# Performance work log

Measured on AMD Instinct MI355X. Metric: run time of the kernel, lower is better.

The kernel has to match this reference:

```python
import jax, jax.numpy as jnp
import numpy as np
from jax import lax

B, L = 4, 1024
D_MODEL, D_STATE, D_CONV = 512, 16, 4
D_INNER = 2 * D_MODEL          # expand=2
DT_RANK = D_MODEL // 16        # ceil(512/16)=32
K_EXPERTS = 2                  # num_experts_per_token; only first k experts are used
EPS = 1e-5


def setup_inputs() -> dict:
    key = jax.random.key(0)
    ks = jax.random.split(key, 14)
    def n(k, shape, scale=0.02):
        return jax.random.normal(k, shape, jnp.float32) * scale
    # Mamba S4D-real init for A: A_log = log(1..d_state) broadcast over channels
    A_log = jnp.log(jnp.broadcast_to(jnp.arange(1, D_STATE + 1, dtype=jnp.float32), (D_INNER, D_STATE)))
    return {
        "x": jax.random.normal(ks[0], (B, L, D_MODEL), jnp.float32),
        "in_proj_w": n(ks[1], (2 * D_INNER, D_MODEL)),
        "conv_w": n(ks[2], (D_INNER, 1, D_CONV), 0.1),
        "conv_b": n(ks[3], (D_INNER,), 0.1),
        "x_proj_w": n(ks[4], (DT_RANK + 2 * D_STATE, D_INNER)),
        "dt_proj_w": n(ks[5], (D_INNER, DT_RANK), 0.1),
        "dt_proj_b": n(ks[6], (D_INNER,), 0.1),
        "A_log": A_log,
        "D_skip": jnp.ones((D_INNER,), jnp.float32),
        "out_proj_w": n(ks[7], (D_MODEL, D_INNER)),
        "moe_w1": n(ks[8], (K_EXPERTS, 2 * D_MODEL, D_MODEL)),
        "moe_b1": n(ks[9], (K_EXPERTS, 2 * D_MODEL)),
        "moe_w2": n(ks[10], (K_EXPERTS, D_MODEL, 2 * D_MODEL)),
        "moe_b2": n(ks[11], (K_EXPERTS, D_MODEL)),
    }


def _layernorm(x):
    # fresh nn.LayerNorm each forward: weight=1, bias=0, eps=1e-5
    mu = jnp.mean(x, -1, keepdims=True)
    var = jnp.mean(jnp.square(x - mu), -1, keepdims=True)
    return (x - mu) / jnp.sqrt(var + EPS)


def _mamba(x, in_proj_w, conv_w, conv_b, x_proj_w, dt_proj_w, dt_proj_b, A_log, D_skip, out_proj_w):
    b = x.shape[0]
    xz = x @ in_proj_w.T                               # (b, L, 2*d_inner)
    xc, z = jnp.split(xz, 2, axis=-1)
    # causal depthwise conv1d (torch pads both sides with d_conv-1 then slices [:L])
    conv = lax.conv_general_dilated(
        xc.transpose(0, 2, 1), conv_w, (1,), [(D_CONV - 1, 0)],
        feature_group_count=D_INNER) + conv_b[None, :, None]
    xs = jax.nn.silu(conv).transpose(0, 2, 1)          # (b, L, d_inner)
    dbc = xs @ x_proj_w.T                              # (b, L, dt_rank + 2*d_state)
    dt = dbc[..., :DT_RANK]
    Bm = dbc[..., DT_RANK:DT_RANK + D_STATE]           # (b, L, d_state)
    Cm = dbc[..., DT_RANK + D_STATE:]                  # (b, L, d_state)
    delta = jax.nn.softplus(dt @ dt_proj_w.T + dt_proj_b)  # (b, L, d_inner)
    A = -jnp.exp(A_log)                                # (d_inner, d_state)
    dA = jnp.exp(jnp.einsum('bld,dn->bldn', delta, A))     # (b, L, d_inner, d_state)
    dBx = (delta * xs)[..., None] * Bm[:, :, None, :]       # (b, L, d_inner, d_state)

    def step(h, inp):
        dA_t, dBx_t, C_t = inp
        h = dA_t * h + dBx_t                           # (b, d_inner, d_state)
        y = jnp.einsum('bdn,bn->bd', h, C_t)
        return h, y

    h0 = jnp.zeros((b, D_INNER, D_STATE), x.dtype)
    _, ys = lax.scan(step, h0, (dA.transpose(1, 0, 2, 3), dBx.transpose(1, 0, 2, 3), Cm.transpose(1, 0, 2)))
    y = ys.transpose(1, 0, 2) + xs * D_skip            # (b, L, d_inner)
    y = y * jax.nn.silu(z)
    return y @ out_proj_w.T                            # (b, L, d_model)


def reference(x, in_proj_w, conv_w, conv_b, x_proj_w, dt_proj_w, dt_proj_b,
              A_log, D_skip, out_proj_w, moe_w1, moe_b1, moe_w2, moe_b2):
    skip = x
    h = _layernorm(x)
    h = _mamba(h, in_proj_w, conv_w, conv_b, x_proj_w, dt_proj_w, dt_proj_b, A_log, D_skip, out_proj_w) + h
    h = _layernorm(h)
    # static 'MoE': unweighted average of the first K_EXPERTS dense FFNs
    a = jax.nn.relu(jnp.einsum('bld,ekd->belk', h, moe_w1) + moe_b1[None, :, None, :])
    moe = jnp.einsum('belk,edk->beld', a, moe_w2) + moe_b2[None, :, None, :]
    return jnp.mean(moe, axis=1) + skip
```

## Files before the change

kernel.cpp:

```cpp
#include <hip/hip_runtime.h>
#include <hip/hip_bf16.h>

#define BB 4
#define LL 1024
#define DM 512
#define DI 1024
#define DS 16
#define DTR 32
#define MM (BB*LL)

#define ACT_NONE 0
#define ACT_RELU 1
#define ACT_SP   2

#define CHUNK 128
#define NCH (LL/CHUNK)
#define NSTATE 65536

typedef __attribute__((ext_vector_type(8))) __bf16 bf16x8;
typedef __attribute__((ext_vector_type(8))) unsigned short us8;
typedef __attribute__((ext_vector_type(4))) float f32x4;

__device__ __forceinline__ unsigned short f2bf(float f) {
  union { float f; unsigned int u; } a; a.f = f;
  unsigned int r = a.u + 0x7fffu + ((a.u >> 16) & 1u);
  return (unsigned short)(r >> 16);
}
__device__ __forceinline__ float b2f(unsigned short u) {
  union { unsigned int i; float f; } a; a.i = (unsigned int)u << 16; return a.f;
}

__device__ __forceinline__ bf16x8 ld_frag(const unsigned short* p) {
  us8 s = *(const us8*)p;
  return __builtin_bit_cast(bf16x8, s);
}

__device__ __forceinline__ void gload16(const void* g, void* l) {
  __builtin_amdgcn_global_load_lds(
      (const __attribute__((address_space(1))) void*)g,
      (__attribute__((address_space(3))) void*)l, 16, 0, 0);
}

__global__ __launch_bounds__(256) void prep_kernel(
    const float* __restrict__ in_proj_w, const float* __restrict__ x_proj_w,
    const float* __restrict__ dt_proj_w, const float* __restrict__ out_proj_w,
    const float* __restrict__ moe_w1,    const float* __restrict__ moe_w2,
    const float* __restrict__ moe_b2,
    unsigned short* __restrict__ inpb,  unsigned short* __restrict__ xpjb,
    unsigned short* __restrict__ dtpb,  unsigned short* __restrict__ outpb,
    unsigned short* __restrict__ w1b,   unsigned short* __restrict__ w2cb,
    float* __restrict__ b2avg)
{
  int i = blockIdx.x * 256 + threadIdx.x;
  int i4 = i * 4;
  auto cvt4 = [&](const float* src, unsigned short* dst) {
    float4 v = ((const float4*)src)[i];
    ushort4 o; o.x = f2bf(v.x); o.y = f2bf(v.y); o.z = f2bf(v.z); o.w = f2bf(v.w);
    ((ushort4*)dst)[i] = o;
  };
  if (i4 < 2*DI*DM) cvt4(in_proj_w, inpb);
  if (i4 < 64*DI)   cvt4(x_proj_w, xpjb);
  if (i4 < DI*DTR)  cvt4(dt_proj_w, dtpb);
  if (i4 < DM*DI)   cvt4(out_proj_w, outpb);
  if (i4 < 2*DM*DM*2) cvt4(moe_w1, w1b);
  if (i4 < DM*2*DI) {
    #pragma unroll
    for (int j = 0; j < 4; ++j) {
      int idx = i4 + j;
      int nrow = idx >> 11;
      int t = idx & (2*DI - 1);
      int e = t >> 10;
      int k = t & (DI - 1);
      w2cb[idx] = f2bf(moe_w2[((size_t)e*DM + nrow)*DI + k]);
    }
  }
  if (i4 < DM) {
    #pragma unroll
    for (int j = 0; j < 4; ++j)
      b2avg[i4+j] = 0.5f * (moe_b2[i4+j] + moe_b2[DM + i4+j]);
  }
}

__global__ __launch_bounds__(256) void ln_kernel(const float* __restrict__ in,
                                                 float* __restrict__ outf,
                                                 unsigned short* __restrict__ outb) {
  int row = blockIdx.x;
  const float* p = in + (size_t)row * DM;
  float2 v = ((const float2*)p)[threadIdx.x];
  float s  = v.x + v.y;
  float ss = v.x*v.x + v.y*v.y;
  for (int o = 32; o; o >>= 1) { s += __shfl_down(s, o); ss += __shfl_down(ss, o); }
  __shared__ float red[8];
  int wid = threadIdx.x >> 6, lane = threadIdx.x & 63;
  if (lane == 0) { red[wid] = s; red[4+wid] = ss; }
  __syncthreads();
  s  = red[0]+red[1]+red[2]+red[3];
  ss = red[4]+red[5]+red[6]+red[7];
  float mu = s * (1.f/DM);
  float var = ss * (1.f/DM) - mu*mu;
  float rstd = rsqrtf(var + 1e-5f);
  float2 o2; o2.x = (v.x-mu)*rstd; o2.y = (v.y-mu)*rstd;
  if (outf) ((float2*)(outf + (size_t)row*DM))[threadIdx.x] = o2;
  if (outb) {
    ushort2 u; u.x = f2bf(o2.x); u.y = f2bf(o2.y);
    ((ushort2*)(outb + (size_t)row*DM))[threadIdx.x] = u;
  }
}

template<int BM, int BN, int BK, int WR, int WC, int FM, int FN, int ACT,
         bool OUTF, bool OUTB, bool DBUF>
__global__ __launch_bounds__(256) void gemm_mfma(
    const unsigned short* __restrict__ A, int lda,
    const unsigned short* __restrict__ B, int ldb,
    const float* __restrict__ bias,
    const float* __restrict__ res, int ldres,
    float* __restrict__ Cf, unsigned short* __restrict__ Cb, int ldc,
    int K, float scale, int nbx)
{
  static_assert(WR*WC == 4 && WR*FM*16 == BM && WC*FN*16 == BN, "geom");
  constexpr int ATILE = BM*BK, BTILE = BN*BK;
  constexpr int AL = ATILE/2048, BL = BTILE/2048;
  constexpr bool SWZ = (BK == 64);
  __shared__ unsigned short As[(DBUF?2:1)*ATILE];
  __shared__ unsigned short Bs[(DBUF?2:1)*BTILE];
  const int tid = threadIdx.x;
  const int nwg = gridDim.x;
  const int bid = blockIdx.x;
  const int cpx = nwg >> 3;
  const int wid = ((nwg & 7) == 0) ? ((bid & 7)*cpx + (bid >> 3)) : bid;
  const int bm = (wid / nbx) * BM;
  const int bn = (wid % nbx) * BN;
  const int w = tid >> 6, lane = tid & 63;
  const int wr = w / WC, wc = w % WC;
  const int rl = lane & 15, kg = lane >> 4;

  auto stage = [&](int buf, int k0) {
    #pragma unroll
    for (int it = 0; it < AL; ++it) {
      int o = (it*256 + tid) * 16;
      int os = SWZ ? (o ^ (((o>>7)&7)<<4)) : o;
      int e = os >> 1;
      int r = e / BK, c = e % BK;
      gload16(A + (size_t)(bm + r)*lda + k0 + c, (char*)As + buf*ATILE*2 + o);
    }
    #pragma unroll
    for (int it = 0; it < BL; ++it) {
      int o = (it*256 + tid) * 16;
      int os = SWZ ? (o ^ (((o>>7)&7)<<4)) : o;
      int e = os >> 1;
      int r = e / BK, c = e % BK;
      gload16(B + (size_t)(bn + r)*ldb + k0 + c, (char*)Bs + buf*BTILE*2 + o);
    }
  };

  f32x4 acc[FM][FN];
  #pragma unroll
  for (int m = 0; m < FM; ++m)
    #pragma unroll
    for (int n = 0; n < FN; ++n) { f32x4 z = {0.f,0.f,0.f,0.f}; acc[m][n] = z; }

  auto compute = [&](int buf) {
    #pragma unroll
    for (int kk = 0; kk < BK/32; ++kk) {
      bf16x8 af[FM], bfv[FN];
      #pragma unroll
      for (int m = 0; m < FM; ++m) {
        int byte = ((wr*FM*16 + m*16 + rl)*BK + kk*32 + kg*8) * 2;
        if (SWZ) byte ^= ((byte>>7)&7)<<4;
        af[m] = ld_frag((const unsigned short*)((const char*)As + buf*ATILE*2 + byte));
      }
      #pragma unroll
      for (int n = 0; n < FN; ++n) {
        int byte = ((wc*FN*16 + n*16 + rl)*BK + kk*32 + kg*8) * 2;
        if (SWZ) byte ^= ((byte>>7)&7)<<4;
        bfv[n] = ld_frag((const unsigned short*)((const char*)Bs + buf*BTILE*2 + byte));
      }
      #pragma unroll
      for (int m = 0; m < FM; ++m)
        #pragma unroll
        for (int n = 0; n < FN; ++n)
          acc[m][n] = __builtin_amdgcn_mfma_f32_16x16x32_bf16(af[m], bfv[n], acc[m][n], 0, 0, 0);
    }
  };

  if (DBUF) {
    stage(0, 0);
    const int nk = K / BK;
    for (int it = 0; it < nk; ++it) {
      __syncthreads();
      if (it + 1 < nk) stage((it&1)^1, (it+1)*BK);
      compute(it & 1);
    }
  } else {
    for (int k0 = 0; k0 < K; k0 += BK) {
      stage(0, k0);
      __syncthreads();
      compute(0);
      __syncthreads();
    }
  }

  #pragma unroll
  for (int m = 0; m < FM; ++m) {
    int row = bm + wr*FM*16 + m*16 + kg*4;
    #pragma unroll
    for (int n = 0; n < FN; ++n) {
      int col = bn + wc*FN*16 + n*16 + rl;
      float bv = bias ? bias[col] : 0.f;
      #pragma unroll
      for (int j = 0; j < 4; ++j) {
        float v = acc[m][n][j] * scale + bv;
        if (ACT == ACT_RELU) v = fmaxf(v, 0.f);
        if (ACT == ACT_SP)   v = fmaxf(v, 0.f) + log1pf(__expf(-fabsf(v)));
        if (res) v += res[(size_t)(row + j)*ldres + col];
        size_t off = (size_t)(row + j)*ldc + col;
        if (OUTF) Cf[off] = v;
        if (OUTB) Cb[off] = f2bf(v);
      }
    }
  }
}

__global__ __launch_bounds__(256) void conv_silu_kernel(
    const unsigned short* __restrict__ xzb, const float* __restrict__ conv_w,
    const float* __restrict__ conv_b, unsigned short* __restrict__ xsb)
{
  int t = blockIdx.x * 256 + threadIdx.x;
  int d8 = (t & (DI/8 - 1)) * 8;
  int l = (t >> 7) & (LL-1);
  int b = t >> 17;
  size_t base = (size_t)(b*LL) * 2*DI + d8;
  float acc[8];
  #pragma unroll
  for (int j = 0; j < 8; ++j) acc[j] = conv_b[d8+j];
  #pragma unroll
  for (int k = 0; k < 4; ++k) {
    int ll = l - 3 + k;
    if (ll >= 0) {
      us8 v = *(const us8*)(xzb + base + (size_t)ll * 2*DI);
      #pragma unroll
      for (int j = 0; j < 8; ++j)
        acc[j] = fmaf(conv_w[(d8+j)*4 + k], b2f((unsigned short)v[j]), acc[j]);
    }
  }
  us8 o;
  #pragma unroll
  for (int j = 0; j < 8; ++j) {
    float s = acc[j];
    float v = s / (1.f + __expf(-s));
    o[j] = (unsigned short)f2bf(v);
  }
  *(us8*)(xsb + (size_t)((b*LL + l)*DI) + d8) = o;
}

__global__ __launch_bounds__(256) void scan_p1(
    const unsigned short* __restrict__ deltab,
    const unsigned short* __restrict__ xsb,
    const float* __restrict__ dbc,
    const float* __restrict__ A_log,
    float* __restrict__ P, float* __restrict__ Q)
{
  int blk = blockIdx.x;
  int c  = blk & (NCH-1);
  int dg = (blk >> 3) & 63;
  int b  = blk >> 9;
  int tid = threadIdx.x;
  int g = tid >> 4, n = tid & 15;
  int d0 = dg*16;
  float Adn2 = -__expf(A_log[(d0+g)*DS + n]) * 1.44269504f;
  __shared__ float s_d[16][68], s_dx[16][68], s_B[16][68];
  float h = 0.f, S = 0.f;
  int lbase = c*CHUNK;
  for (int l0 = 0; l0 < CHUNK; l0 += 64) {
    {
      int li = tid >> 2, dd = (tid & 3) * 4;
      size_t row = (size_t)b*LL + lbase + l0 + li;
      ushort4 ud = *(const ushort4*)(deltab + row*DI + d0 + dd);
      ushort4 ux = *(const ushort4*)(xsb    + row*DI + d0 + dd);
      float4 vB = *(const float4*)(dbc   + row*64 + 32 + dd);
      float dx_ = b2f(ud.x), dy_ = b2f(ud.y), dz_ = b2f(ud.z), dw_ = b2f(ud.w);
      float xx_ = b2f(ux.x), xy_ = b2f(ux.y), xz_ = b2f(ux.z), xw_ = b2f(ux.w);
      s_d [dd+0][li]=dx_; s_d [dd+1][li]=dy_; s_d [dd+2][li]=dz_; s_d [dd+3][li]=dw_;
      s_dx[dd+0][li]=dx_*xx_; s_dx[dd+1][li]=dy_*xy_; s_dx[dd+2][li]=dz_*xz_; s_dx[dd+3][li]=dw_*xw_;
      s_B [dd+0][li]=vB.x; s_B [dd+1][li]=vB.y; s_B [dd+2][li]=vB.z; s_B [dd+3][li]=vB.w;
    }
    __syncthreads();
    #pragma unroll
    for (int q4 = 0; q4 < 64; q4 += 4) {
      float4 vd  = *(const float4*)&s_d[g][q4];
      float4 vdx = *(const float4*)&s_dx[g][q4];
      float4 vB  = *(const float4*)&s_B[n][q4];
      float dA;
      dA = exp2f(vd.x*Adn2); h = fmaf(dA, h, vdx.x*vB.x); S += vd.x;
      dA = exp2f(vd.y*Adn2); h = fmaf(dA, h, vdx.y*vB.y); S += vd.y;
      dA = exp2f(vd.z*Adn2); h = fmaf(dA, h, vdx.z*vB.z); S += vd.z;
      dA = exp2f(vd.w*Adn2); h = fmaf(dA, h, vdx.w*vB.w); S += vd.w;
    }
    __syncthreads();
  }
  int base = ((b*64 + dg)*256 + g*16 + n) + NSTATE*c;
  P[base] = exp2f(S * Adn2);
  Q[base] = h;
}

__global__ __launch_bounds__(256) void scan_stitch(
    const float* __restrict__ P, const float* __restrict__ Q,
    float* __restrict__ H)
{
  int t = blockIdx.x * 256 + threadIdx.x;
  float h = 0.f;
  #pragma unroll
  for (int c = 0; c < NCH; ++c) {
    H[t + NSTATE*c] = h;
    h = fmaf(P[t + NSTATE*c], h, Q[t + NSTATE*c]);
  }
}

__global__ __launch_bounds__(256) void scan_p2(
    const unsigned short* __restrict__ deltab,
    const unsigned short* __restrict__ xsb,
    const unsigned short* __restrict__ xzb,
    const float* __restrict__ dbc,
    const float* __restrict__ A_log,
    const float* __restrict__ D_skip,
    const float* __restrict__ H,
    unsigned short* __restrict__ ymulb)
{
  int blk = blockIdx.x;
  int c  = blk & (NCH-1);
  int dg = (blk >> 3) & 63;
  int b  = blk >> 9;
  int tid = threadIdx.x;
  int g = tid >> 4, n = tid & 15;
  int d0 = dg*16;
  float Adn2 = -__expf(A_log[(d0+g)*DS + n]) * 1.44269504f;
  __shared__ float s_d[16][68], s_dx[16][68], s_B[16][68], s_C[16][68];
  __shared__ float s_z[64][17], s_t[64][17];
  __shared__ float s_yp[16][16][17];
  float h = H[((b*64 + dg)*256 + g*16 + n) + NSTATE*c];
  int lbase = c*CHUNK;
  for (int l0 = 0; l0 < CHUNK; l0 += 64) {
    {
      int li = tid >> 2, dd = (tid & 3) * 4;
      size_t row = (size_t)b*LL + lbase + l0 + li;
      ushort4 ud = *(const ushort4*)(deltab + row*DI + d0 + dd);
      ushort4 ux = *(const ushort4*)(xsb    + row*DI + d0 + dd);
      ushort4 uz = *(const ushort4*)(xzb    + row*2*DI + DI + d0 + dd);
      float4 vB = *(const float4*)(dbc   + row*64 + 32 + dd);
      float4 vC = *(const float4*)(dbc   + row*64 + 48 + dd);
      float4 vD = *(const float4*)(D_skip + d0 + dd);
      float dx_ = b2f(ud.x), dy_ = b2f(ud.y), dz_ = b2f(ud.z), dw_ = b2f(ud.w);
      float xx_ = b2f(ux.x), xy_ = b2f(ux.y), xz2 = b2f(ux.z), xw_ = b2f(ux.w);
      float zx_ = b2f(uz.x), zy_ = b2f(uz.y), zz_ = b2f(uz.z), zw_ = b2f(uz.w);
      s_d [dd+0][li]=dx_; s_d [dd+1][li]=dy_; s_d [dd+2][li]=dz_; s_d [dd+3][li]=dw_;
      s_dx[dd+0][li]=dx_*xx_; s_dx[dd+1][li]=dy_*xy_; s_dx[dd+2][li]=dz_*xz2; s_dx[dd+3][li]=dw_*xw_;
      s_B [dd+0][li]=vB.x; s_B [dd+1][li]=vB.y; s_B [dd+2][li]=vB.z; s_B [dd+3][li]=vB.w;
      s_C [dd+0][li]=vC.x; s_C [dd+1][li]=vC.y; s_C [dd+2][li]=vC.z; s_C [dd+3][li]=vC.w;
      float szx = zx_ / (1.f + __expf(-zx_));
      float szy = zy_ / (1.f + __expf(-zy_));
      float szz = zz_ / (1.f + __expf(-zz_));
      float szw = zw_ / (1.f + __expf(-zw_));
      s_z[li][dd+0]=szx; s_z[li][dd+1]=szy; s_z[li][dd+2]=szz; s_z[li][dd+3]=szw;
      s_t[li][dd+0]=xx_*vD.x*szx; s_t[li][dd+1]=xy_*vD.y*szy;
      s_t[li][dd+2]=xz2*vD.z*szz; s_t[li][dd+3]=xw_*vD.w*szw;
    }
    __syncthreads();
    #pragma unroll
    for (int sub = 0; sub < 4; ++sub) {
      #pragma unroll
      for (int q4 = 0; q4 < 16; q4 += 4) {
        int li = sub*16 + q4;
        float4 vd  = *(const float4*)&s_d[g][li];
        float4 vdx = *(const float4*)&s_dx[g][li];
        float4 vB  = *(const float4*)&s_B[n][li];
        float4 vC  = *(const float4*)&s_C[n][li];
        float dA;
        dA = exp2f(vd.x*Adn2); h = fmaf(dA, h, vdx.x*vB.x); s_yp[g][n][q4+0] = h*vC.x;
        dA = exp2f(vd.y*Adn2); h = fmaf(dA, h, vdx.y*vB.y); s_yp[g][n][q4+1] = h*vC.y;
        dA = exp2f(vd.z*Adn2); h = fmaf(dA, h, vdx.z*vB.z); s_yp[g][n][q4+2] = h*vC.z;
        dA = exp2f(vd.w*Adn2); h = fmaf(dA, h, vdx.w*vB.w); s_yp[g][n][q4+3] = h*vC.w;
      }
      __syncthreads();
      {
        int q_r = tid & 15, g_r = tid >> 4;
        float y = 0.f;
        #pragma unroll
        for (int nn = 0; nn < 16; ++nn) y += s_yp[g_r][nn][q_r];
        int lis = sub*16 + q_r;
        float v = y * s_z[lis][g_r] + s_t[lis][g_r];
        ymulb[((size_t)b*LL + lbase + l0 + lis)*DI + d0 + g_r] = f2bf(v);
      }
      __syncthreads();
    }
  }
}

extern "C" void kernel_launch(void* const* d_in, const int* in_sizes, int n_in,
                              void* d_out, int out_size, void* d_ws, size_t ws_size,
                              hipStream_t stream) {
  const float* x         = (const float*)d_in[0];
  const float* in_proj_w = (const float*)d_in[1];
  const float* conv_w    = (const float*)d_in[2];
  const float* conv_b    = (const float*)d_in[3];
  const float* x_proj_w  = (const float*)d_in[4];
  const float* dt_proj_w = (const float*)d_in[5];
  const float* dt_proj_b = (const float*)d_in[6];
  const float* A_log     = (const float*)d_in[7];
  const float* D_skip    = (const float*)d_in[8];
  const float* out_proj_w= (const float*)d_in[9];
  const float* moe_w1    = (const float*)d_in[10];
  const float* moe_b1    = (const float*)d_in[11];
  const float* moe_w2    = (const float*)d_in[12];
  const float* moe_b2    = (const float*)d_in[13];
  float* out = (float*)d_out;

  float* p = (float*)d_ws;
  float* h1    = p; p += 2097152;
  float* h2    = p; p += 2097152;
  float* dbc   = p; p += 262144;
  float* Pbuf  = p; p += NSTATE*NCH/1;
  float* Qbuf  = p; p += 524288;
  float* Hbuf  = p; p += 524288;
  float* b2avg = p; p += 1024;
  unsigned short* h1b    = (unsigned short*)p; p += 1048576;
  unsigned short* xzb    = (unsigned short*)p; p += 4194304;
  unsigned short* xsb    = (unsigned short*)p; p += 2097152;
  unsigned short* deltab = (unsigned short*)p; p += 2097152;
  unsigned short* dbcb   = (unsigned short*)p; p += 131072;
  unsigned short* ymulb  = (unsigned short*)p; p += 2097152;
  unsigned short* h2lnb  = (unsigned short*)p; p += 1048576;
  unsigned short* acatb  = (unsigned short*)p; p += 4194304;
  unsigned short* inpb   = (unsigned short*)p; p += 524288;
  unsigned short* xpjb   = (unsigned short*)p; p += 32768;
  unsigned short* dtpb   = (unsigned short*)p; p += 16384;
  unsigned short* outpb  = (unsigned short*)p; p += 262144;
  unsigned short* w1b    = (unsigned short*)p; p += 524288;
  unsigned short* w2cb   = (unsigned short*)p; p += 524288;

  prep_kernel<<<1024, 256, 0, stream>>>(in_proj_w, x_proj_w, dt_proj_w, out_proj_w,
                                        moe_w1, moe_w2, moe_b2,
                                        inpb, xpjb, dtpb, outpb, w1b, w2cb, b2avg);
  ln_kernel<<<MM, 256, 0, stream>>>(x, h1, h1b);
  gemm_mfma<128,128,64,2,2,4,4,ACT_NONE,false,true,true><<<512, 256, 0, stream>>>(
      h1b, DM, inpb, DM, nullptr, nullptr, 0, nullptr, xzb, 2*DI, DM, 1.f, 16);
  conv_silu_kernel<<<(MM*DI/8)/256, 256, 0, stream>>>(xzb, conv_w, conv_b, xsb);
  gemm_mfma<64,64,64,2,2,2,2,ACT_NONE,true,true,true><<<64, 256, 0, stream>>>(
      xsb, DI, xpjb, DI, nullptr, nullptr, 0, dbc, dbcb, 64, DI, 1.f, 1);
  gemm_mfma<128,128,32,2,2,4,4,ACT_SP,false,true,false><<<256, 256, 0, stream>>>(
      dbcb, 64, dtpb, DTR, dt_proj_b, nullptr, 0, nullptr, deltab, DI, DTR, 1.f, 8);
  scan_p1<<<BB*64*NCH, 256, 0, stream>>>(deltab, xsb, dbc, A_log, Pbuf, Qbuf);
  scan_stitch<<<NSTATE/256, 256, 0, stream>>>(Pbuf, Qbuf, Hbuf);
  scan_p2<<<BB*64*NCH, 256, 0, stream>>>(deltab, xsb, xzb, dbc, A_log, D_skip, Hbuf, ymulb);
  gemm_mfma<64,64,64,2,2,2,2,ACT_NONE,true,false,true><<<512, 256, 0, stream>>>(
      ymulb, DI, outpb, DI, nullptr, h1, DM, h2, nullptr, DM, DI, 1.f, 8);
  ln_kernel<<<MM, 256, 0, stream>>>(h2, nullptr, h2lnb);
  gemm_mfma<128,128,64,2,2,4,4,ACT_RELU,false,true,true><<<512, 256, 0, stream>>>(
      h2lnb, DM, w1b, DM, moe_b1, nullptr, 0, nullptr, acatb, 2*DI, DM, 1.f, 16);
  gemm_mfma<64,64,64,2,2,2,2,ACT_NONE,true,false,true><<<512, 256, 0, stream>>>(
      acatb, 2*DI, w2cb, 2*DI, b2avg, x, DM, out, nullptr, DM, 2*DI, 0.5f, 8);
}
```

Baseline: 221.4 us.

## Fuse dt_proj+softplus into scan pass, merge prep with layernorm, drop stitch kernel

The dt_proj GEMM with softplus is folded into scan_p1: each block computes delta for its 16 channels from dbc and dt_proj_w held in shared memory, and writes deltab for scan_p2. The scan_stitch kernel is removed, so each scan_p2 block rebuilds its starting state by walking the preceding chunk P/Q values itself. The weight-prep kernel and the first layernorm become one launch. The GEMM pipeline now always double-buffers, using explicit vmcnt waits and barriers to overlap the next tile's loads with compute. Together these cut launches and intermediate traffic, at the cost of some redundant prefix work in scan_p2 and more shared memory in scan_p1.

```diff
diff --git a/kernel.cpp b/kernel.cpp
--- a/kernel.cpp
+++ b/kernel.cpp
@@ -11,7 +11,6 @@
 
 #define ACT_NONE 0
 #define ACT_RELU 1
-#define ACT_SP   2
 
 #define CHUNK 128
 #define NCH (LL/CHUNK)
@@ -41,17 +40,42 @@
       (__attribute__((address_space(3))) void*)l, 16, 0, 0);
 }
 
-__global__ __launch_bounds__(256) void prep_kernel(
+__global__ __launch_bounds__(256) void prep_ln_kernel(
+    const float* __restrict__ x,
     const float* __restrict__ in_proj_w, const float* __restrict__ x_proj_w,
-    const float* __restrict__ dt_proj_w, const float* __restrict__ out_proj_w,
+    const float* __restrict__ out_proj_w,
     const float* __restrict__ moe_w1,    const float* __restrict__ moe_w2,
     const float* __restrict__ moe_b2,
+    float* __restrict__ h1, unsigned short* __restrict__ h1b,
     unsigned short* __restrict__ inpb,  unsigned short* __restrict__ xpjb,
-    unsigned short* __restrict__ dtpb,  unsigned short* __restrict__ outpb,
+    unsigned short* __restrict__ outpb,
     unsigned short* __restrict__ w1b,   unsigned short* __restrict__ w2cb,
     float* __restrict__ b2avg)
 {
-  int i = blockIdx.x * 256 + threadIdx.x;
+  __shared__ float red[8];
+  int bid = blockIdx.x;
+  if (bid < MM) {
+    int row = bid;
+    const float* p = x + (size_t)row * DM;
+    float2 v = ((const float2*)p)[threadIdx.x];
+    float s  = v.x + v.y;
+    float ss = v.x*v.x + v.y*v.y;
+    for (int o = 32; o; o >>= 1) { s += __shfl_down(s, o); ss += __shfl_down(ss, o); }
+    int wid = threadIdx.x >> 6, lane = threadIdx.x & 63;
+    if (lane == 0) { red[wid] = s; red[4+wid] = ss; }
+    __syncthreads();
+    s  = red[0]+red[1]+red[2]+red[3];
+    ss = red[4]+red[5]+red[6]+red[7];
+    float mu = s * (1.f/DM);
+    float var = ss * (1.f/DM) - mu*mu;
+    float rstd = rsqrtf(var + 1e-5f);
+    float2 o2; o2.x = (v.x-mu)*rstd; o2.y = (v.y-mu)*rstd;
+    ((float2*)(h1 + (size_t)row*DM))[threadIdx.x] = o2;
+    ushort2 u; u.x = f2bf(o2.x); u.y = f2bf(o2.y);
+    ((ushort2*)(h1b + (size_t)row*DM))[threadIdx.x] = u;
+    return;
+  }
+  int i = (bid - MM) * 256 + threadIdx.x;
   int i4 = i * 4;
   auto cvt4 = [&](const float* src, unsigned short* dst) {
     float4 v = ((const float4*)src)[i];
@@ -60,9 +84,8 @@
   };
   if (i4 < 2*DI*DM) cvt4(in_proj_w, inpb);
   if (i4 < 64*DI)   cvt4(x_proj_w, xpjb);
-  if (i4 < DI*DTR)  cvt4(dt_proj_w, dtpb);
   if (i4 < DM*DI)   cvt4(out_proj_w, outpb);
-  if (i4 < 2*DM*DM*2) cvt4(moe_w1, w1b);
+  if (i4 < 2*(2*DM)*DM) cvt4(moe_w1, w1b);
   if (i4 < DM*2*DI) {
     #pragma unroll
     for (int j = 0; j < 4; ++j) {
@@ -108,7 +131,7 @@
 }
 
 template<int BM, int BN, int BK, int WR, int WC, int FM, int FN, int ACT,
-         bool OUTF, bool OUTB, bool DBUF>
+         bool OUTF, bool OUTB>
 __global__ __launch_bounds__(256) void gemm_mfma(
     const unsigned short* __restrict__ A, int lda,
     const unsigned short* __restrict__ B, int ldb,
@@ -121,8 +144,8 @@
   constexpr int ATILE = BM*BK, BTILE = BN*BK;
   constexpr int AL = ATILE/2048, BL = BTILE/2048;
   constexpr bool SWZ = (BK == 64);
-  __shared__ unsigned short As[(DBUF?2:1)*ATILE];
-  __shared__ unsigned short Bs[(DBUF?2:1)*BTILE];
+  __shared__ unsigned short As[2*ATILE];
+  __shared__ unsigned short Bs[2*BTILE];
   const int tid = threadIdx.x;
   const int nwg = gridDim.x;
   const int bid = blockIdx.x;
@@ -183,21 +206,18 @@
     }
   };
 
-  if (DBUF) {
-    stage(0, 0);
-    const int nk = K / BK;
-    for (int it = 0; it < nk; ++it) {
-      __syncthreads();
-      if (it + 1 < nk) stage((it&1)^1, (it+1)*BK);
-      compute(it & 1);
-    }
-  } else {
-    for (int k0 = 0; k0 < K; k0 += BK) {
-      stage(0, k0);
-      __syncthreads();
-      compute(0);
-      __syncthreads();
-    }
+  stage(0, 0);
+  const int nk = K / BK;
+  for (int it = 0; it < nk; ++it) {
+    if (it + 1 < nk) {
+      stage((it&1)^1, (it+1)*BK);
+      asm volatile("s_waitcnt vmcnt(%0)" :: "i"(AL+BL) : "memory");
+    } else {
+      asm volatile("s_waitcnt vmcnt(0)" ::: "memory");
+    }
+    __builtin_amdgcn_s_barrier();
+    compute(it & 1);
+    __builtin_amdgcn_s_barrier();
   }
 
   #pragma unroll
@@ -211,7 +231,6 @@
       for (int j = 0; j < 4; ++j) {
         float v = acc[m][n][j] * scale + bv;
         if (ACT == ACT_RELU) v = fmaxf(v, 0.f);
-        if (ACT == ACT_SP)   v = fmaxf(v, 0.f) + log1pf(__expf(-fabsf(v)));
         if (res) v += res[(size_t)(row + j)*ldres + col];
         size_t off = (size_t)(row + j)*ldc + col;
         if (OUTF) Cf[off] = v;
@@ -254,11 +273,13 @@
 }
 
 __global__ __launch_bounds__(256) void scan_p1(
-    const unsigned short* __restrict__ deltab,
+    const float* __restrict__ dbc,
     const unsigned short* __restrict__ xsb,
-    const float* __restrict__ dbc,
+    const float* __restrict__ dtw,
+    const float* __restrict__ dtb,
     const float* __restrict__ A_log,
-    float* __restrict__ P, float* __restrict__ Q)
+    float* __restrict__ P, float* __restrict__ Q,
+    unsigned short* __restrict__ deltab)
 {
   int blk = blockIdx.x;
   int c  = blk & (NCH-1);
@@ -269,20 +290,55 @@
   int d0 = dg*16;
   float Adn2 = -__expf(A_log[(d0+g)*DS + n]) * 1.44269504f;
   __shared__ float s_d[16][68], s_dx[16][68], s_B[16][68];
+  __shared__ float s_dt[64][33];
+  __shared__ float s_w[16][32];
+  __shared__ float s_bs[16];
+  {
+    int dr = tid >> 5, jc = tid & 31;
+    s_w[dr][jc]   = dtw[(d0+dr)*DTR + jc];
+    s_w[dr+8][jc] = dtw[(d0+dr+8)*DTR + jc];
+    if (tid < 16) s_bs[tid] = dtb[d0 + tid];
+  }
   float h = 0.f, S = 0.f;
   int lbase = c*CHUNK;
   for (int l0 = 0; l0 < CHUNK; l0 += 64) {
     {
       int li = tid >> 2, dd = (tid & 3) * 4;
       size_t row = (size_t)b*LL + lbase + l0 + li;
-      ushort4 ud = *(const ushort4*)(deltab + row*DI + d0 + dd);
-      ushort4 ux = *(const ushort4*)(xsb    + row*DI + d0 + dd);
-      float4 vB = *(const float4*)(dbc   + row*64 + 32 + dd);
-      float dx_ = b2f(ud.x), dy_ = b2f(ud.y), dz_ = b2f(ud.z), dw_ = b2f(ud.w);
-      float xx_ = b2f(ux.x), xy_ = b2f(ux.y), xz_ = b2f(ux.z), xw_ = b2f(ux.w);
-      s_d [dd+0][li]=dx_; s_d [dd+1][li]=dy_; s_d [dd+2][li]=dz_; s_d [dd+3][li]=dw_;
-      s_dx[dd+0][li]=dx_*xx_; s_dx[dd+1][li]=dy_*xy_; s_dx[dd+2][li]=dz_*xz_; s_dx[dd+3][li]=dw_*xw_;
+      ushort4 ux = *(const ushort4*)(xsb + row*DI + d0 + dd);
+      float4 vB = *(const float4*)(dbc + row*64 + 32 + dd);
+      float4 t0 = *(const float4*)(dbc + row*64 + dd);
+      float4 t1 = *(const float4*)(dbc + row*64 + 16 + dd);
+      s_dx[dd+0][li]=b2f(ux.x); s_dx[dd+1][li]=b2f(ux.y);
+      s_dx[dd+2][li]=b2f(ux.z); s_dx[dd+3][li]=b2f(ux.w);
       s_B [dd+0][li]=vB.x; s_B [dd+1][li]=vB.y; s_B [dd+2][li]=vB.z; s_B [dd+3][li]=vB.w;
+      *(float4*)&s_dt[li][dd]      = t0;
+      *(float4*)&s_dt[li][16 + dd] = t1;
+    }
+    __syncthreads();
+    {
+      int l = tid & 63, dq = tid >> 6;
+      size_t row = (size_t)b*LL + lbase + l0 + l;
+      ushort4 dout;
+      #pragma unroll
+      for (int k = 0; k < 4; ++k) {
+        int d = dq*4 + k;
+        float acc = s_bs[d];
+        #pragma unroll
+        for (int j = 0; j < 32; j += 4) {
+          float4 wt  = *(const float4*)&s_w[d][j];
+          float4 dt4 = *(const float4*)&s_dt[l][j];
+          acc = fmaf(wt.x, dt4.x, acc); acc = fmaf(wt.y, dt4.y, acc);
+          acc = fmaf(wt.z, dt4.z, acc); acc = fmaf(wt.w, dt4.w, acc);
+        }
+        float sp = fmaxf(acc, 0.f) + log1pf(__expf(-fabsf(acc)));
+        unsigned short spb = f2bf(sp);
+        float spf = b2f(spb);
+        ((unsigned short*)&dout)[k] = spb;
+        s_d[d][l] = spf;
+        s_dx[d][l] *= spf;
+      }
+      *(ushort4*)(deltab + row*DI + d0 + dq*4) = dout;
     }
     __syncthreads();
     #pragma unroll
@@ -303,19 +359,6 @@
   Q[base] = h;
 }
 
-__global__ __launch_bounds__(256) void scan_stitch(
-    const float* __restrict__ P, const float* __restrict__ Q,
-    float* __restrict__ H)
-{
-  int t = blockIdx.x * 256 + threadIdx.x;
-  float h = 0.f;
-  #pragma unroll
-  for (int c = 0; c < NCH; ++c) {
-    H[t + NSTATE*c] = h;
-    h = fmaf(P[t + NSTATE*c], h, Q[t + NSTATE*c]);
-  }
-}
-
 __global__ __launch_bounds__(256) void scan_p2(
     const unsigned short* __restrict__ deltab,
     const unsigned short* __restrict__ xsb,
@@ -323,7 +366,7 @@
     const float* __restrict__ dbc,
     const float* __restrict__ A_log,
     const float* __restrict__ D_skip,
-    const float* __restrict__ H,
+    const float* __restrict__ P, const float* __restrict__ Q,
     unsigned short* __restrict__ ymulb)
 {
   int blk = blockIdx.x;
@@ -337,7 +380,12 @@
   __shared__ float s_d[16][68], s_dx[16][68], s_B[16][68], s_C[16][68];
   __shared__ float s_z[64][17], s_t[64][17];
   __shared__ float s_yp[16][16][17];
-  float h = H[((b*64 + dg)*256 + g*16 + n) + NSTATE*c];
+  float h = 0.f;
+  {
+    int t = (b*64 + dg)*256 + g*16 + n;
+    for (int cc = 0; cc < c; ++cc)
+      h = fmaf(P[t + NSTATE*cc], h, Q[t + NSTATE*cc]);
+  }
   int lbase = c*CHUNK;
   for (int l0 = 0; l0 < CHUNK; l0 += 64) {
     {
@@ -418,44 +466,39 @@
   float* h1    = p; p += 2097152;
   float* h2    = p; p += 2097152;
   float* dbc   = p; p += 262144;
-  float* Pbuf  = p; p += NSTATE*NCH/1;
+  float* Pbuf  = p; p += 524288;
   float* Qbuf  = p; p += 524288;
-  float* Hbuf  = p; p += 524288;
   float* b2avg = p; p += 1024;
   unsigned short* h1b    = (unsigned short*)p; p += 1048576;
   unsigned short* xzb    = (unsigned short*)p; p += 4194304;
   unsigned short* xsb    = (unsigned short*)p; p += 2097152;
   unsigned short* deltab = (unsigned short*)p; p += 2097152;
-  unsigned short* dbcb   = (unsigned short*)p; p += 131072;
   unsigned short* ymulb  = (unsigned short*)p; p += 2097152;
   unsigned short* h2lnb  = (unsigned short*)p; p += 1048576;
   unsigned short* acatb  = (unsigned short*)p; p += 4194304;
   unsigned short* inpb   = (unsigned short*)p; p += 524288;
   unsigned short* xpjb   = (unsigned short*)p; p += 32768;
-  unsigned short* dtpb   = (unsigned short*)p; p += 16384;
   unsigned short* outpb  = (unsigned short*)p; p += 262144;
   unsigned short* w1b    = (unsigned short*)p; p += 524288;
   unsigned short* w2cb   = (unsigned short*)p; p += 524288;
 
-  prep_kernel<<<1024, 256, 0, stream>>>(in_proj_w, x_proj_w, dt_proj_w, out_proj_w,
-                                        moe_w1, moe_w2, moe_b2,
-                                        inpb, xpjb, dtpb, outpb, w1b, w2cb, b2avg);
-  ln_kernel<<<MM, 256, 0, stream>>>(x, h1, h1b);
-  gemm_mfma<128,128,64,2,2,4,4,ACT_NONE,false,true,true><<<512, 256, 0, stream>>>(
+  prep_ln_kernel<<<MM + 1024, 256, 0, stream>>>(x, in_proj_w, x_proj_w, out_proj_w,
+                                                moe_w1, moe_w2, moe_b2,
+                                                h1, h1b, inpb, xpjb, outpb, w1b, w2cb, b2avg);
+  gemm_mfma<128,128,64,2,2,4,4,ACT_NONE,false,true><<<512, 256, 0, stream>>>(
       h1b, DM, inpb, DM, nullptr, nullptr, 0, nullptr, xzb, 2*DI, DM, 1.f, 16);
   conv_silu_kernel<<<(MM*DI/8)/256, 256, 0, stream>>>(xzb, conv_w, conv_b, xsb);
-  gemm_mfma<64,64,64,2,2,2,2,ACT_NONE,true,true,true><<<64, 256, 0, stream>>>(
-      xsb, DI, xpjb, DI, nullptr, nullptr, 0, dbc, dbcb, 64, DI, 1.f, 1);
-  gemm_mfma<128,128,32,2,2,4,4,ACT_SP,false,true,false><<<256, 256, 0, stream>>>(
-      dbcb, 64, dtpb, DTR, dt_proj_b, nullptr, 0, nullptr, deltab, DI, DTR, 1.f, 8);
-  scan_p1<<<BB*64*NCH, 256, 0, stream>>>(deltab, xsb, dbc, A_log, Pbuf, Qbuf);
-  scan_stitch<<<NSTATE/256, 256, 0, stream>>>(Pbuf, Qbuf, Hbuf);
-  scan_p2<<<BB*64*NCH, 256, 0, stream>>>(deltab, xsb, xzb, dbc, A_log, D_skip, Hbuf, ymulb);
-  gemm_mfma<64,64,64,2,2,2,2,ACT_NONE,true,false,true><<<512, 256, 0, stream>>>(
+  gemm_mfma<64,64,64,2,2,2,2,ACT_NONE,true,false><<<64, 256, 0, stream>>>(
+      xsb, DI, xpjb, DI, nullptr, nullptr, 0, dbc, nullptr, 64, DI, 1.f, 1);
+  scan_p1<<<BB*64*NCH, 256, 0, stream>>>(dbc, xsb, dt_proj_w, dt_proj_b, A_log,
+                                         Pbuf, Qbuf, deltab);
+  scan_p2<<<BB*64*NCH, 256, 0, stream>>>(deltab, xsb, xzb, dbc, A_log, D_skip,
+                                         Pbuf, Qbuf, ymulb);
+  gemm_mfma<64,64,64,2,2,2,2,ACT_NONE,true,false><<<512, 256, 0, stream>>>(
       ymulb, DI, outpb, DI, nullptr, h1, DM, h2, nullptr, DM, DI, 1.f, 8);
   ln_kernel<<<MM, 256, 0, stream>>>(h2, nullptr, h2lnb);
-  gemm_mfma<128,128,64,2,2,4,4,ACT_RELU,false,true,true><<<512, 256, 0, stream>>>(
+  gemm_mfma<128,128,64,2,2,4,4,ACT_RELU,false,true><<<512, 256, 0, stream>>>(
       h2lnb, DM, w1b, DM, moe_b1, nullptr, 0, nullptr, acatb, 2*DI, DM, 1.f, 16);
-  gemm_mfma<64,64,64,2,2,2,2,ACT_NONE,true,false,true><<<512, 256, 0, stream>>>(
+  gemm_mfma<64,64,64,2,2,2,2,ACT_NONE,true,false><<<512, 256, 0, stream>>>(
       acatb, 2*DI, w2cb, 2*DI, b2avg, x, DM, out, nullptr, DM, 2*DI, 0.5f, 8);
 }
```

After: 211.0 us. 1.05x faster.
